# Performance work log

Hardware: AMD Instinct MI355X
Metric: run time of the kernel (lower is better)

## Reference

```python
import jax, jax.numpy as jnp
import numpy as np

IN_DIM = 64
OUT_DIM = 64
ATTN_DIM = 5
N_REL = 200
N_ENT = 40000
N_NODE = 500000
N_EDGE = 1000000
BATCH = 32


def setup_inputs() -> dict:
    key = jax.random.key(0)
    ks = jax.random.split(key, 20)
    n_rel_emb = 2 * N_REL + 1
    # forward args
    q_sub = jax.random.randint(ks[0], (BATCH,), 0, N_ENT)
    q_rel = jax.random.randint(ks[1], (BATCH,), 0, n_rel_emb)
    hidden = jax.random.normal(ks[2], (N_NODE, IN_DIM), dtype=jnp.float32)
    # edges columns: 0=batch idx, 1=unused, 2=rel, 3=unused, 4=sub, 5=obj
    e_batch = jax.random.randint(ks[3], (N_EDGE,), 0, BATCH)
    e_rel = jax.random.randint(ks[4], (N_EDGE,), 0, n_rel_emb)
    e_sub = jax.random.randint(ks[5], (N_EDGE,), 0, N_NODE)
    e_obj = jax.random.randint(ks[6], (N_EDGE,), 0, N_NODE)
    edges = jnp.stack([e_batch, e_batch, e_rel, e_rel, e_sub, e_obj], axis=1)
    nodes = jnp.stack([jax.random.randint(ks[7], (N_NODE,), 0, BATCH),
                       jax.random.randint(ks[8], (N_NODE,), 0, N_ENT)], axis=1)
    old_nodes_new_idx = jax.random.randint(ks[9], (100000,), 0, N_NODE)
    # parameters (stored as [in, out]; torch Linear does x @ W.T + b)
    def lin(k, fan_in, fan_out):
        b = 1.0 / np.sqrt(fan_in)
        return jax.random.uniform(k, (fan_in, fan_out), jnp.float32, -b, b)
    rela_embed = jax.random.normal(ks[10], (n_rel_emb, IN_DIM), dtype=jnp.float32)
    return {
        "hidden": hidden,
        "rela_embed": rela_embed,
        "Ws": lin(ks[11], IN_DIM, ATTN_DIM),
        "Wr": lin(ks[12], IN_DIM, ATTN_DIM),
        "Wqr_w": lin(ks[13], IN_DIM, ATTN_DIM),
        "Wqr_b": jnp.zeros((ATTN_DIM,), jnp.float32),
        "walpha_w": lin(ks[14], ATTN_DIM, 1),
        "walpha_b": jnp.zeros((1,), jnp.float32),
        "Wh": lin(ks[15], IN_DIM, OUT_DIM),
        "attn_fc_w": lin(ks[16], 2 * OUT_DIM, 1),
        "attn_fc_b": jnp.zeros((1,), jnp.float32),
        "Wnode_w": lin(ks[17], OUT_DIM, OUT_DIM),
        "Wnode_b": jnp.zeros((OUT_DIM,), jnp.float32),
        "q_sub": q_sub,
        "q_rel": q_rel,
        "edges": edges,
        "nodes": nodes,
        "old_nodes_new_idx": old_nodes_new_idx,
        "batchsize": BATCH,
    }


def reference(hidden, rela_embed, Ws, Wr, Wqr_w, Wqr_b, walpha_w, walpha_b,
              Wh, attn_fc_w, attn_fc_b, Wnode_w, Wnode_b,
              q_sub, q_rel, edges, nodes, old_nodes_new_idx, batchsize):
    n_node = nodes.shape[0]
    r_idx, rel, sub, obj = edges[:, 0], edges[:, 2], edges[:, 4], edges[:, 5]
    hs = hidden[sub]                      # [E, in_dim] gather
    hr = rela_embed[rel]                  # [E, in_dim]
    h_qr = rela_embed[q_rel][r_idx]       # [E, in_dim]
    message = hs - hr                     # [E, in_dim]
    attn = jax.nn.relu(hs @ Ws + hr @ Wr + h_qr @ Wqr_w + Wqr_b)   # [E, attn_dim]
    alpha = jax.nn.sigmoid(attn @ walpha_w + walpha_b)             # [E, 1]
    message = alpha * message
    # scatter-max over obj; empty segments filled with 0 (torch_scatter semantics)
    agg = jax.ops.segment_max(message, obj, num_segments=n_node)   # [n_node, in_dim]
    agg = jnp.where(jnp.isneginf(agg), 0.0, agg)
    hidden_new = agg @ Wh                 # act = identity        [n_node, out_dim]
    # edge attention over new node states
    cat = jnp.concatenate([hidden_new[sub], hidden_new[obj]], axis=-1)  # [E, 2*out]
    scores = jax.nn.leaky_relu((cat @ attn_fc_w + attn_fc_b)[:, 0], 0.2)  # [E]
    # source code overwrites scatter_softmax with a global softmax over all edges
    w = jax.nn.softmax(scores)            # [E]
    msg2 = w[:, None] * (hidden_new[obj] @ Wnode_w + Wnode_b)      # [E, out_dim]
    hidden_new = jax.ops.segment_sum(msg2, sub, num_segments=n_node)
    return hidden_new
```

## Files before the change

### kernel.cpp

```cpp
#include <hip/hip_runtime.h>
#include <math.h>
#include <float.h>


#define SCAN_BLK 256
#define SCAN_ITEMS 4
#define SCAN_CHUNK (SCAN_BLK * SCAN_ITEMS)
#define SOFT_G 2048
#define NPW 8

__global__ void k_tables(const float* __restrict__ rela, const float* __restrict__ Wr,
                         const float* __restrict__ Wqr_w, const float* __restrict__ Wqr_b,
                         const int* __restrict__ q_rel,
                         float* __restrict__ s2, float* __restrict__ s3,
                         int nrel, int batch) {
  int tid = blockIdx.x * blockDim.x + threadIdx.x;
  int stride = gridDim.x * blockDim.x;
  for (int idx = tid; idx < nrel * 5; idx += stride) {
    int r = idx / 5, j = idx % 5;
    float acc = 0.f;
    for (int k = 0; k < 64; k++) acc += rela[r * 64 + k] * Wr[k * 5 + j];
    s2[idx] = acc;
  }
  for (int idx = tid; idx < batch * 5; idx += stride) {
    int b = idx / 5, j = idx % 5;
    int qr = q_rel[b];
    float acc = Wqr_b[j];
    for (int k = 0; k < 64; k++) acc += rela[qr * 64 + k] * Wqr_w[k * 5 + j];
    s3[idx] = acc;
  }
}

__global__ void k_fuse(const float* __restrict__ Wh, const float* __restrict__ Wn,
                       const float* __restrict__ fw,
                       float* __restrict__ W2, float* __restrict__ fuv) {
  int tid = threadIdx.x;
  for (int idx = tid; idx < 64 * 64; idx += 256) {
    int k = idx >> 6, m = idx & 63;
    float acc = 0.f;
    for (int j = 0; j < 64; j++) acc += Wh[k * 64 + j] * Wn[j * 64 + m];
    W2[idx] = acc;
  }
  if (tid < 128) {
    int k = tid & 63, h = tid >> 6;
    float acc = 0.f;
    for (int j = 0; j < 64; j++) acc += Wh[k * 64 + j] * fw[h * 64 + j];
    fuv[h * 64 + k] = acc;
  }
}

__global__ void __launch_bounds__(256, 2)
k_proj(const float* __restrict__ hidden, const float* __restrict__ Ws_g,
       float* __restrict__ P, int N) {
  int n = blockIdx.x * blockDim.x + threadIdx.x;
  if (n >= N) return;
  float hs[64];
  const float4* h4 = (const float4*)(hidden + (size_t)n * 64);
#pragma unroll
  for (int k4 = 0; k4 < 16; k4++) {
    float4 h = h4[k4];
    hs[k4 * 4 + 0] = h.x; hs[k4 * 4 + 1] = h.y; hs[k4 * 4 + 2] = h.z; hs[k4 * 4 + 3] = h.w;
  }
  float acc[5] = {0.f, 0.f, 0.f, 0.f, 0.f};
#pragma unroll
  for (int k = 0; k < 64; k++) {
    float h = hs[k];
#pragma unroll
    for (int j = 0; j < 5; j++) acc[j] += h * Ws_g[k * 5 + j];
  }
#pragma unroll
  for (int j = 0; j < 5; j++) P[(size_t)n * 5 + j] = acc[j];
}

__global__ void k_hist(const int* __restrict__ edges, int* __restrict__ cnt, int E, int N) {
  int e = blockIdx.x * blockDim.x + threadIdx.x;
  if (e < E) {
    int sub = edges[e * 6 + 4];
    int obj = edges[e * 6 + 5];
    atomicAdd(&cnt[obj], 1);
    atomicAdd(&cnt[N + sub], 1);
  }
}

__global__ void k_scan_partial(const int* __restrict__ cnt, int* __restrict__ part, int n) {
  __shared__ int sdata[SCAN_BLK];
  int base = blockIdx.x * SCAN_CHUNK + threadIdx.x * SCAN_ITEMS;
  int s = 0;
#pragma unroll
  for (int j = 0; j < SCAN_ITEMS; j++) { int i = base + j; if (i < n) s += cnt[i]; }
  sdata[threadIdx.x] = s;
  __syncthreads();
  for (int d = SCAN_BLK / 2; d > 0; d >>= 1) {
    if (threadIdx.x < d) sdata[threadIdx.x] += sdata[threadIdx.x + d];
    __syncthreads();
  }
  if (threadIdx.x == 0) part[blockIdx.x] = sdata[0];
}

__global__ void k_scan_top(int* part, int nblk) {
  __shared__ int lds[1024];
  int tid = threadIdx.x;
  int v = (tid < nblk) ? part[tid] : 0;
  lds[tid] = v;
  __syncthreads();
  for (int d = 1; d < 1024; d <<= 1) {
    int t = (tid >= d) ? lds[tid - d] : 0;
    __syncthreads();
    lds[tid] += t;
    __syncthreads();
  }
  if (tid < nblk) part[tid] = lds[tid] - v;
}

__global__ void k_scan_final(const int* __restrict__ cnt, const int* __restrict__ part,
                             int* __restrict__ off, int n) {
  __shared__ int lds[SCAN_BLK];
  int tid = threadIdx.x;
  int base = blockIdx.x * SCAN_CHUNK + tid * SCAN_ITEMS;
  int c[SCAN_ITEMS];
  int s = 0;
#pragma unroll
  for (int j = 0; j < SCAN_ITEMS; j++) { int i = base + j; c[j] = (i < n) ? cnt[i] : 0; s += c[j]; }
  int v = s;
  lds[tid] = s;
  __syncthreads();
  for (int d = 1; d < SCAN_BLK; d <<= 1) {
    int t = (tid >= d) ? lds[tid - d] : 0;
    __syncthreads();
    lds[tid] += t;
    __syncthreads();
  }
  int run = part[blockIdx.x] + (lds[tid] - v);
#pragma unroll
  for (int j = 0; j < SCAN_ITEMS; j++) { int i = base + j; if (i < n) off[i] = run; run += c[j]; }
}

__global__ void k_scatter(const int* __restrict__ edges, const float* __restrict__ P,
                          const float* __restrict__ s2, const float* __restrict__ s3,
                          const float* __restrict__ walpha_w, const float* __restrict__ walpha_b,
                          int* __restrict__ cur, int4* __restrict__ rec_obj,
                          int2* __restrict__ rec_sub, int E, int N) {
  int e = blockIdx.x * blockDim.x + threadIdx.x;
  if (e >= E) return;
  int ridx = edges[e * 6 + 0];
  int rel  = edges[e * 6 + 2];
  int sub  = edges[e * 6 + 4];
  int obj  = edges[e * 6 + 5];
  float z = walpha_b[0];
#pragma unroll
  for (int j = 0; j < 5; j++) {
    float vj = P[(size_t)sub * 5 + j] + s2[rel * 5 + j] + s3[ridx * 5 + j];
    z += fmaxf(vj, 0.f) * walpha_w[j];
  }
  float a = 1.f / (1.f + expf(-z));
  int p = atomicAdd(&cur[obj], 1);
  rec_obj[p] = make_int4(sub, rel, __float_as_int(a), 0);
  int q = atomicAdd(&cur[N + sub], 1) - E;
  rec_sub[q] = make_int2(obj, sub);
}

__global__ void __launch_bounds__(256, 4)
k_agg2(const int* __restrict__ off, const int4* __restrict__ rec_obj,
       const float* __restrict__ hidden, const float* __restrict__ rela,
       const float* __restrict__ W2, const float* __restrict__ fuv,
       float* __restrict__ agg2, float* __restrict__ u, float* __restrict__ v,
       int N) {
  __shared__ float w2s[64 * 64];
  __shared__ float rows[4][NPW][64];
  for (int idx = threadIdx.x; idx < 1024; idx += 256)
    ((float4*)w2s)[idx] = ((const float4*)W2)[idx];
  __syncthreads();
  int lane  = threadIdx.x & 63;
  int wslot = threadIdx.x >> 6;
  int wid   = blockIdx.x * (blockDim.x >> 6) + wslot;
  int node0 = wid * NPW;
  if (node0 >= N) return;
  float fu = fuv[lane], fv = fuv[64 + lane];
  int ov = 0;
  if (lane <= NPW) {
    int idx = node0 + lane;
    if (idx > N) idx = N;
    ov = off[idx];
  }
  int B   = __shfl(ov, 0);
  int End = __shfl(ov, NPW);
  int lbase = B;
  int rx = 0, ry = 0; float rz = 0.f;
  {
    int p = lbase + lane;
    if (p < End) { int4 r = rec_obj[p]; rx = r.x; ry = r.y; rz = __int_as_float(r.z); }
  }
  int cur = B;
  for (int i = 0; i < NPW; i++) {
    int node = node0 + i;
    if (node >= N) break;
    int en = __shfl(ov, i + 1);
    int bst = cur;
    float vmax = -FLT_MAX;
    while (cur < en) {
      int idx = cur - lbase;
      if (idx >= 64) {
        lbase += 64;
        int p = lbase + lane;
        if (p < End) { int4 r = rec_obj[p]; rx = r.x; ry = r.y; rz = __int_as_float(r.z); }
        idx = 0;
      }
      int sub = __shfl(rx, idx);
      int rel = __shfl(ry, idx);
      float a = __shfl(rz, idx);
      float x = a * (hidden[(size_t)sub * 64 + lane] - rela[rel * 64 + lane]);
      vmax = fmaxf(vmax, x);
      cur++;
    }
    float rowv = (en > bst) ? vmax : 0.f;
    rows[wslot][i][lane] = rowv;
    float ur = rowv * fu, vr = rowv * fv;
#pragma unroll
    for (int m = 32; m > 0; m >>= 1) {
      ur += __shfl_xor(ur, m);
      vr += __shfl_xor(vr, m);
    }
    if (lane == 0) { u[node] = ur; v[node] = vr; }
  }
  int nv = min(NPW, N - node0);
  float acc[NPW];
#pragma unroll
  for (int i = 0; i < NPW; i++) acc[i] = 0.f;
  for (int k4 = 0; k4 < 16; k4++) {
    float w0 = w2s[(k4 * 4 + 0) * 64 + lane];
    float w1 = w2s[(k4 * 4 + 1) * 64 + lane];
    float w2 = w2s[(k4 * 4 + 2) * 64 + lane];
    float w3 = w2s[(k4 * 4 + 3) * 64 + lane];
#pragma unroll
    for (int i = 0; i < NPW; i++) {
      float4 r4 = *(const float4*)&rows[wslot][i][k4 * 4];
      acc[i] = fmaf(r4.x, w0, fmaf(r4.y, w1, fmaf(r4.z, w2, fmaf(r4.w, w3, acc[i]))));
    }
  }
  for (int i = 0; i < nv; i++)
    agg2[(size_t)(node0 + i) * 64 + lane] = acc[i];
}

__global__ void k_scores(const int2* __restrict__ rec_sub, const float* __restrict__ u,
                         const float* __restrict__ v, const float* __restrict__ fb,
                         float* __restrict__ scores, float* __restrict__ pmax,
                         float* __restrict__ psum, int E) {
  __shared__ float red_m[256], red_s[256];
  float b = fb[0];
  float lm = -FLT_MAX, ls = 0.f;
  for (int pos = blockIdx.x * blockDim.x + threadIdx.x; pos < E; pos += gridDim.x * blockDim.x) {
    int2 r = rec_sub[pos];
    float s = u[r.y] + v[r.x] + b;
    s = (s >= 0.f) ? s : 0.2f * s;
    scores[pos] = s;
    if (s > lm) { ls = ls * expf(lm - s) + 1.f; lm = s; }
    else        { ls += expf(s - lm); }
  }
  red_m[threadIdx.x] = lm; red_s[threadIdx.x] = ls;
  __syncthreads();
  for (int d = blockDim.x / 2; d > 0; d >>= 1) {
    if (threadIdx.x < d) {
      float m1 = red_m[threadIdx.x], s1 = red_s[threadIdx.x];
      float m2 = red_m[threadIdx.x + d], s2 = red_s[threadIdx.x + d];
      float m = fmaxf(m1, m2);
      float s = 0.f;
      if (m > -FLT_MAX) s = s1 * expf(m1 - m) + s2 * expf(m2 - m);
      red_m[threadIdx.x] = m; red_s[threadIdx.x] = s;
    }
    __syncthreads();
  }
  if (threadIdx.x == 0) { pmax[blockIdx.x] = red_m[0]; psum[blockIdx.x] = red_s[0]; }
}

__global__ void k_softmax_final(const float* __restrict__ pmax, const float* __restrict__ psum,
                                float* __restrict__ scal, int G) {
  __shared__ float red_m[256], red_s[256];
  float lm = -FLT_MAX, ls = 0.f;
  for (int i = threadIdx.x; i < G; i += 256) {
    float m2 = pmax[i], s2 = psum[i];
    if (m2 > lm) { ls = ls * expf(lm - m2) + s2; lm = m2; }
    else         { ls += s2 * expf(m2 - lm); }
  }
  red_m[threadIdx.x] = lm; red_s[threadIdx.x] = ls;
  __syncthreads();
  for (int d = 128; d > 0; d >>= 1) {
    if (threadIdx.x < d) {
      float m1 = red_m[threadIdx.x], s1 = red_s[threadIdx.x];
      float m2 = red_m[threadIdx.x + d], s2 = red_s[threadIdx.x + d];
      float m = fmaxf(m1, m2);
      float s = 0.f;
      if (m > -FLT_MAX) s = s1 * expf(m1 - m) + s2 * expf(m2 - m);
      red_m[threadIdx.x] = m; red_s[threadIdx.x] = s;
    }
    __syncthreads();
  }
  if (threadIdx.x == 0) { scal[0] = red_m[0]; scal[1] = red_s[0]; }
}

__global__ void k_expw(float* __restrict__ scores, const float* __restrict__ scal, int E) {
  int i = blockIdx.x * blockDim.x + threadIdx.x;
  if (i < E) scores[i] = expf(scores[i] - scal[0]);
}

__global__ void k_aggsum(const int* __restrict__ off, const int2* __restrict__ rec_sub,
                         const float* __restrict__ wexp, const float* __restrict__ agg2,
                         const float* __restrict__ bias, const float* __restrict__ scal,
                         float* __restrict__ out, int N, int E) {
  int lane = threadIdx.x & 63;
  int wid  = blockIdx.x * (blockDim.x >> 6) + (threadIdx.x >> 6);
  int node0 = wid * NPW;
  if (node0 >= N) return;
  float bl = bias[lane];
  float inv = 1.f / scal[1];
  int ov = 0;
  if (lane <= NPW) {
    int idx = node0 + lane;
    ov = (idx >= N) ? E : (off[N + idx] - E);
  }
  int B   = __shfl(ov, 0);
  int End = __shfl(ov, NPW);
  int lbase = B;
  int objr = 0; float wr = 0.f;
  {
    int p = lbase + lane;
    if (p < End) { objr = rec_sub[p].x; wr = wexp[p]; }
  }
  int cur = B;
  for (int i = 0; i < NPW; i++) {
    int node = node0 + i;
    if (node >= N) break;
    int en = __shfl(ov, i + 1);
    float acc = 0.f, wa = 0.f;
    while (cur < en) {
      int idx = cur - lbase;
      if (idx >= 64) {
        lbase += 64;
        int p = lbase + lane;
        if (p < End) { objr = rec_sub[p].x; wr = wexp[p]; }
        idx = 0;
      }
      int obj = __shfl(objr, idx);
      float ww = __shfl(wr, idx);
      acc += ww * agg2[(size_t)obj * 64 + lane];
      wa  += ww;
      cur++;
    }
    out[(size_t)node * 64 + lane] = (acc + wa * bl) * inv;
  }
}

extern "C" void kernel_launch(void* const* d_in, const int* in_sizes, int n_in,
                              void* d_out, int out_size, void* d_ws, size_t ws_size,
                              hipStream_t stream) {
  const float* hidden    = (const float*)d_in[0];
  const float* rela      = (const float*)d_in[1];
  const float* Ws        = (const float*)d_in[2];
  const float* Wr        = (const float*)d_in[3];
  const float* Wqr_w     = (const float*)d_in[4];
  const float* Wqr_b     = (const float*)d_in[5];
  const float* walpha_w  = (const float*)d_in[6];
  const float* walpha_b  = (const float*)d_in[7];
  const float* Wh        = (const float*)d_in[8];
  const float* attn_fc_w = (const float*)d_in[9];
  const float* attn_fc_b = (const float*)d_in[10];
  const float* Wnode_w   = (const float*)d_in[11];
  const float* Wnode_b   = (const float*)d_in[12];
  const int*   q_rel     = (const int*)d_in[14];
  const int*   edges     = (const int*)d_in[15];

  int N = in_sizes[0] / 64;
  int E = in_sizes[15] / 6;
  int nrel = in_sizes[1] / 64;
  int batch = in_sizes[14];

  char* w = (char*)d_ws;
  size_t o = 0;
  #define WS_ALLOC(ptr_t, name, bytes) \
    ptr_t name = (ptr_t)(w + o); o = (o + (size_t)(bytes) + 255) & ~(size_t)255;
  WS_ALLOC(float*, agg2,    (size_t)N * 64 * 4)
  WS_ALLOC(float*, P,       (size_t)N * 5 * 4)
  WS_ALLOC(int4*,  rec_obj, (size_t)E * 16)
  WS_ALLOC(int2*,  rec_sub, (size_t)E * 8)
  WS_ALLOC(int*,   cnt,     (size_t)2 * N * 4)
  WS_ALLOC(int*,   off,     (size_t)2 * N * 4)
  WS_ALLOC(int*,   part,    1024 * 4)
  WS_ALLOC(float*, pmax,    SOFT_G * 4)
  WS_ALLOC(float*, psum,    SOFT_G * 4)
  WS_ALLOC(float*, s2t,     (size_t)nrel * 5 * 4)
  WS_ALLOC(float*, s3t,     (size_t)batch * 5 * 4)
  WS_ALLOC(float*, scal,    2 * 4)
  WS_ALLOC(float*, W2,      64 * 64 * 4)
  WS_ALLOC(float*, fuv,     2 * 64 * 4)
  #undef WS_ALLOC

  float* u = P;
  float* v = P + N;
  float* scores = (float*)cnt;

  k_tables<<<16, 256, 0, stream>>>(rela, Wr, Wqr_w, Wqr_b, q_rel, s2t, s3t, nrel, batch);
  k_fuse<<<1, 256, 0, stream>>>(Wh, Wnode_w, attn_fc_w, W2, fuv);
  k_proj<<<(N + 255) / 256, 256, 0, stream>>>(hidden, Ws, P, N);
  hipMemsetAsync(cnt, 0, (size_t)2 * N * 4, stream);
  k_hist<<<(E + 255) / 256, 256, 0, stream>>>(edges, cnt, E, N);
  int SCAN_N = 2 * N;
  int nblk = (SCAN_N + SCAN_CHUNK - 1) / SCAN_CHUNK;
  k_scan_partial<<<nblk, SCAN_BLK, 0, stream>>>(cnt, part, SCAN_N);
  k_scan_top<<<1, 1024, 0, stream>>>(part, nblk);
  k_scan_final<<<nblk, SCAN_BLK, 0, stream>>>(cnt, part, off, SCAN_N);
  hipMemcpyAsync(cnt, off, (size_t)2 * N * 4, hipMemcpyDeviceToDevice, stream);
  k_scatter<<<(E + 255) / 256, 256, 0, stream>>>(edges, P, s2t, s3t, walpha_w, walpha_b,
                                                 cnt, rec_obj, rec_sub, E, N);
  int csr_blocks = (N + NPW * 4 - 1) / (NPW * 4);
  k_agg2<<<csr_blocks, 256, 0, stream>>>(off, rec_obj, hidden, rela, W2, fuv,
                                         agg2, u, v, N);
  k_scores<<<SOFT_G, 256, 0, stream>>>(rec_sub, u, v, attn_fc_b, scores, pmax, psum, E);
  k_softmax_final<<<1, 256, 0, stream>>>(pmax, psum, scal, SOFT_G);
  k_expw<<<(E + 255) / 256, 256, 0, stream>>>(scores, scal, E);
  k_aggsum<<<csr_blocks, 256, 0, stream>>>(off, rec_sub, scores , agg2,
                                           Wnode_b, scal, (float*)d_out, N, E);
}
```

Measured before the change: 822.6 us.

## Unroll CSR gather loops by four and fold exp weighting into aggsum

Result: no change. 830.3 us (+0.9%).

```diff
diff --git a/kernel.cpp b/kernel.cpp
--- a/kernel.cpp
+++ b/kernel.cpp
@@ -205,12 +205,27 @@
         if (p < End) { int4 r = rec_obj[p]; rx = r.x; ry = r.y; rz = __int_as_float(r.z); }
         idx = 0;
       }
-      int sub = __shfl(rx, idx);
-      int rel = __shfl(ry, idx);
-      float a = __shfl(rz, idx);
-      float x = a * (hidden[(size_t)sub * 64 + lane] - rela[rel * 64 + lane]);
-      vmax = fmaxf(vmax, x);
-      cur++;
+      int c = min(min(en - cur, 64 - idx), 4);
+      int i1 = idx + ((c > 1) ? 1 : 0);
+      int i2 = idx + ((c > 2) ? 2 : 0);
+      int i3 = idx + ((c > 3) ? 3 : 0);
+      int s0 = __shfl(rx, idx); int g0 = __shfl(ry, idx); float a0 = __shfl(rz, idx);
+      int s1 = __shfl(rx, i1);  int g1 = __shfl(ry, i1);  float a1 = __shfl(rz, i1);
+      int s2 = __shfl(rx, i2);  int g2 = __shfl(ry, i2);  float a2 = __shfl(rz, i2);
+      int s3 = __shfl(rx, i3);  int g3 = __shfl(ry, i3);  float a3 = __shfl(rz, i3);
+      float h0 = hidden[(size_t)s0 * 64 + lane];
+      float h1 = hidden[(size_t)s1 * 64 + lane];
+      float h2 = hidden[(size_t)s2 * 64 + lane];
+      float h3 = hidden[(size_t)s3 * 64 + lane];
+      float e0 = rela[g0 * 64 + lane];
+      float e1 = rela[g1 * 64 + lane];
+      float e2 = rela[g2 * 64 + lane];
+      float e3 = rela[g3 * 64 + lane];
+      vmax = fmaxf(vmax, a0 * (h0 - e0));
+      if (c > 1) vmax = fmaxf(vmax, a1 * (h1 - e1));
+      if (c > 2) vmax = fmaxf(vmax, a2 * (h2 - e2));
+      if (c > 3) vmax = fmaxf(vmax, a3 * (h3 - e3));
+      cur += c;
     }
     float rowv = (en > bst) ? vmax : 0.f;
     rows[wslot][i][lane] = rowv;
@@ -297,13 +312,8 @@
   if (threadIdx.x == 0) { scal[0] = red_m[0]; scal[1] = red_s[0]; }
 }
 
-__global__ void k_expw(float* __restrict__ scores, const float* __restrict__ scal, int E) {
-  int i = blockIdx.x * blockDim.x + threadIdx.x;
-  if (i < E) scores[i] = expf(scores[i] - scal[0]);
-}
-
 __global__ void k_aggsum(const int* __restrict__ off, const int2* __restrict__ rec_sub,
-                         const float* __restrict__ wexp, const float* __restrict__ agg2,
+                         const float* __restrict__ scores, const float* __restrict__ agg2,
                          const float* __restrict__ bias, const float* __restrict__ scal,
                          float* __restrict__ out, int N, int E) {
   int lane = threadIdx.x & 63;
@@ -311,6 +321,7 @@
   int node0 = wid * NPW;
   if (node0 >= N) return;
   float bl = bias[lane];
+  float gmax = scal[0];
   float inv = 1.f / scal[1];
   int ov = 0;
   if (lane <= NPW) {
@@ -323,7 +334,7 @@
   int objr = 0; float wr = 0.f;
   {
     int p = lbase + lane;
-    if (p < End) { objr = rec_sub[p].x; wr = wexp[p]; }
+    if (p < End) { objr = rec_sub[p].x; wr = expf(scores[p] - gmax); }
   }
   int cur = B;
   for (int i = 0; i < NPW; i++) {
@@ -336,14 +347,26 @@
       if (idx >= 64) {
         lbase += 64;
         int p = lbase + lane;
-        if (p < End) { objr = rec_sub[p].x; wr = wexp[p]; }
+        if (p < End) { objr = rec_sub[p].x; wr = expf(scores[p] - gmax); }
         idx = 0;
       }
-      int obj = __shfl(objr, idx);
-      float ww = __shfl(wr, idx);
-      acc += ww * agg2[(size_t)obj * 64 + lane];
-      wa  += ww;
-      cur++;
+      int c = min(min(en - cur, 64 - idx), 4);
+      int i1 = idx + ((c > 1) ? 1 : 0);
+      int i2 = idx + ((c > 2) ? 2 : 0);
+      int i3 = idx + ((c > 3) ? 3 : 0);
+      int o0 = __shfl(objr, idx); float w0 = __shfl(wr, idx);
+      int o1 = __shfl(objr, i1);  float w1 = __shfl(wr, i1);
+      int o2 = __shfl(objr, i2);  float w2 = __shfl(wr, i2);
+      int o3 = __shfl(objr, i3);  float w3 = __shfl(wr, i3);
+      float h0 = agg2[(size_t)o0 * 64 + lane];
+      float h1 = agg2[(size_t)o1 * 64 + lane];
+      float h2 = agg2[(size_t)o2 * 64 + lane];
+      float h3 = agg2[(size_t)o3 * 64 + lane];
+      acc += w0 * h0; wa += w0;
+      if (c > 1) { acc += w1 * h1; wa += w1; }
+      if (c > 2) { acc += w2 * h2; wa += w2; }
+      if (c > 3) { acc += w3 * h3; wa += w3; }
+      cur += c;
     }
     out[(size_t)node * 64 + lane] = (acc + wa * bl) * inv;
   }
@@ -415,7 +438,6 @@
                                          agg2, u, v, N);
   k_scores<<<SOFT_G, 256, 0, stream>>>(rec_sub, u, v, attn_fc_b, scores, pmax, psum, E);
   k_softmax_final<<<1, 256, 0, stream>>>(pmax, psum, scal, SOFT_G);
-  k_expw<<<(E + 255) / 256, 256, 0, stream>>>(scores, scal, E);
-  k_aggsum<<<csr_blocks, 256, 0, stream>>>(off, rec_sub, scores , agg2,
+  k_aggsum<<<csr_blocks, 256, 0, stream>>>(off, rec_sub, scores, agg2,
                                            Wnode_b, scal, (float*)d_out, N, E);
 }
```
